# Performance work log

Measured on AMD Instinct MI355X. Metric: run time of the kernel, lower is better.

## Reference

```python
import jax, jax.numpy as jnp
import numpy as np


def setup_inputs() -> dict:
    key = jax.random.key(0)
    k0, k1, k2, k3, k4 = jax.random.split(key, 5)
    B, W, C, C2, D = 4, 64, 512, 512, 64  # D = C // k, k=8
    x = jax.random.normal(k0, (B, W, W, C), dtype=jnp.float32)
    input_h = jax.random.normal(k1, (B, W, W, C2), dtype=jnp.float32)
    f = jax.random.normal(k2, (1, 1, C2, D), dtype=jnp.float32) * 0.02
    g = jax.random.normal(k3, (1, 1, C, D), dtype=jnp.float32) * 0.02
    gamma = jax.random.uniform(k4, (1,), dtype=jnp.float32)
    return {"x": x, "input_h": input_h, "f": f, "g": g, "gamma": gamma}


def reference(x, input_h, f, g, gamma):
    # x: [B,W,W,C] NHWC, input_h: [B,W,W,C2], f: [1,1,C2,D], g: [1,1,C,D]
    B, W, _, C = x.shape
    C2 = input_h.shape[-1]
    N = W * W
    # 1x1 convs == per-pixel channel matmuls
    f_proj = jnp.einsum('bhwc,cd->bhwd', input_h, f[0, 0])  # [B,W,W,D]
    g_proj = jnp.einsum('bhwc,cd->bhwd', x, g[0, 0])        # [B,W,W,D]
    f_flat = f_proj.reshape(B, N, -1)
    g_flat = g_proj.reshape(B, N, -1)
    # unscaled attention scores over spatial positions
    s = jnp.einsum('bnd,bmd->bnm', g_flat, f_flat)          # [B,N,N]
    beta = jax.nn.softmax(s, axis=-1)
    h_flat = input_h.reshape(B, N, C2)
    o = jnp.einsum('bnm,bmc->bnc', beta, h_flat).reshape(B, W, W, C2)
    # mix_concat == 'mix': learned residual mix
    return gamma * o + x
```

## Files before the change

### kernel.cpp

```cpp
#include <hip/hip_runtime.h>
#include <hip/hip_bf16.h>
#include <cstdint>
#include <cstddef>


#define NPOS 4096
#define CCH  512
#define DQK  64
#define LSTR 72

typedef __attribute__((ext_vector_type(8)))  short s8v;
typedef __attribute__((ext_vector_type(4)))  short s4v;
typedef __attribute__((ext_vector_type(4)))  float f4v;

__device__ __forceinline__ float bf2f(unsigned short u) {
    unsigned int x = ((unsigned int)u) << 16;
    return __builtin_bit_cast(float, x);
}
__device__ __forceinline__ unsigned short f2bf(float f) {
    unsigned int u = __builtin_bit_cast(unsigned int, f);
    u += 0x7fffu + ((u >> 16) & 1u);
    return (unsigned short)(u >> 16);
}

__global__ __launch_bounds__(256) void wt_kernel(
    const float* __restrict__ f, const float* __restrict__ g,
    unsigned short* __restrict__ fT, unsigned short* __restrict__ gT)
{
    int gid = blockIdx.x * 256 + threadIdx.x;
    for (int e = 0; e < 4; ++e) {
        int i = e * 16384 + gid;
        int which = i >> 15;
        int j = i & 32767;
        int d = j >> 9, k = j & 511;
        const float* s = which ? g : f;
        unsigned short* dst = which ? gT : fT;
        dst[j] = f2bf(s[k * 64 + d]);
    }
}

__global__ __launch_bounds__(256) void vt_kernel(
    const float* __restrict__ ih, unsigned short* __restrict__ Vt)
{
    __shared__ unsigned short T[64 * 65];
    const int tid = threadIdx.x;
    const int bidx = blockIdx.x;
    const int bb = bidx >> 9;
    const int rem = bidx & 511;
    const int ct = rem >> 6;
    const int nt = rem & 63;

    for (int p = 0; p < 4; ++p) {
        int idx = p * 256 + tid;
        int r = idx >> 4, gg = idx & 15;
        f4v v = *(const f4v*)(ih + ((size_t)bb * NPOS + nt * 64 + r) * CCH + ct * 64 + gg * 4);
        for (int j = 0; j < 4; ++j) T[r * 65 + gg * 4 + j] = f2bf(v[j]);
    }
    __syncthreads();
    for (int p = 0; p < 2; ++p) {
        int idx = p * 256 + tid;
        int c = idx >> 3, ng = idx & 7;
        unsigned short tmp[8];
        for (int j = 0; j < 8; ++j) tmp[j] = T[(ng * 8 + j) * 65 + c];
        *(s8v*)(Vt + ((size_t)bb * CCH + ct * 64 + c) * NPOS + nt * 64 + ng * 8) = *(const s8v*)tmp;
    }
}

__global__ __launch_bounds__(256) void proj_kernel(
    const float* __restrict__ x,  const float* __restrict__ ih,
    const unsigned short* __restrict__ gT, const unsigned short* __restrict__ fT,
    unsigned short* __restrict__ Qg, unsigned short* __restrict__ Kf)
{
    __shared__ __align__(16) short Alds[128 * LSTR];
    __shared__ __align__(16) short Wlds[64 * LSTR];
    const int tid = threadIdx.x;
    const int wave = tid >> 6, lane = tid & 63;
    const int n15 = lane & 15, quad = lane >> 4;
    const int which = blockIdx.x >> 7;
    const int rb = (blockIdx.x & 127) * 128;
    const float* src = which ? ih : x;
    const unsigned short* wT  = which ? fT : gT;
    unsigned short* dst = which ? Kf : Qg;

    f4v acc[2][4];
    for (int i = 0; i < 2; ++i)
        for (int j = 0; j < 4; ++j)
            acc[i][j] = f4v{0.f, 0.f, 0.f, 0.f};

    for (int kc = 0; kc < 8; ++kc) {
        for (int p = 0; p < 8; ++p) {
            int idx = p * 256 + tid;
            int r = idx >> 4, gg = idx & 15;
            f4v v = *(const f4v*)(src + (size_t)(rb + r) * CCH + kc * 64 + gg * 4);
            s4v tv;
            for (int j = 0; j < 4; ++j) tv[j] = (short)f2bf(v[j]);
            *(s4v*)&Alds[r * LSTR + gg * 4] = tv;
        }
        for (int p = 0; p < 2; ++p) {
            int idx = p * 256 + tid;
            int c = idx >> 3, gg = idx & 7;
            *(s8v*)&Wlds[c * LSTR + gg * 8] =
                *(const s8v*)(wT + (size_t)c * CCH + kc * 64 + gg * 8);
        }
        __syncthreads();
        for (int kk = 0; kk < 2; ++kk) {
            s8v af0 = *(const s8v*)&Alds[(wave * 32 +      n15) * LSTR + kk * 32 + quad * 8];
            s8v af1 = *(const s8v*)&Alds[(wave * 32 + 16 + n15) * LSTR + kk * 32 + quad * 8];
            for (int ct = 0; ct < 4; ++ct) {
                s8v bf = *(const s8v*)&Wlds[(ct * 16 + n15) * LSTR + kk * 32 + quad * 8];
                acc[0][ct] = __builtin_amdgcn_mfma_f32_16x16x32_bf16(af0, bf, acc[0][ct], 0, 0, 0);
                acc[1][ct] = __builtin_amdgcn_mfma_f32_16x16x32_bf16(af1, bf, acc[1][ct], 0, 0, 0);
            }
        }
        __syncthreads();
    }
    for (int rt = 0; rt < 2; ++rt)
        for (int ct = 0; ct < 4; ++ct)
            for (int r = 0; r < 4; ++r) {
                int row = wave * 32 + rt * 16 + quad * 4 + r;
                int col = ct * 16 + n15;
                dst[(size_t)(rb + row) * DQK + col] = f2bf(acc[rt][ct][r]);
            }
}

__global__ __launch_bounds__(512) void flash_kernel(
    const unsigned short* __restrict__ Qg,
    const unsigned short* __restrict__ Kf,
    const unsigned short* __restrict__ Vt,
    const float* __restrict__ xin,
    const float* __restrict__ gptr,
    float* __restrict__ out)
{
    __shared__ __align__(16) short Klds[2 * 64 * LSTR];
    __shared__ __align__(16) short Plds[64 * LSTR];
    __shared__ float l_s[64];

    const int tid = threadIdx.x;
    const int wave = tid >> 6;
    const int lane = tid & 63;
    const int n15 = lane & 15, quad = lane >> 4;
    const int bid = blockIdx.x;
    const int xcd = bid & 7;
    const int b = xcd >> 1;
    const int qt = (xcd & 1) + ((bid >> 3) << 1);
    const int qbase = qt * 64;

    const float SOFT_M = 20.0f;
    float lpart = 0.0f;

    f4v acc[4][4];
    for (int i = 0; i < 4; ++i)
        for (int j = 0; j < 4; ++j)
            acc[i][j] = f4v{0.f, 0.f, 0.f, 0.f};

    const int ti = wave >> 1;
    const int mi0 = (wave & 1) * 2;
    s8v qf[2];
    {
        const unsigned short* qp =
            Qg + ((size_t)b * NPOS + qbase + ti * 16 + n15) * DQK + quad * 8;
        qf[0] = *(const s8v*)(qp);
        qf[1] = *(const s8v*)(qp + 32);
    }

    const int cb = wave * 64;
    const unsigned short* Vb = Vt + (size_t)b * CCH * NPOS;

    const int kr = tid >> 3, kg = tid & 7;
    const unsigned short* kbase_p = Kf + ((size_t)b * NPOS + kr) * DQK + kg * 8;
    s8v kreg = *(const s8v*)(kbase_p);

    for (int kb = 0; kb < NPOS / 64; ++kb) {
        const int m0 = kb * 64;
        *(s8v*)&Klds[(kb & 1) * 64 * LSTR + kr * LSTR + kg * 8] = kreg;
        if (kb + 1 < NPOS / 64)
            kreg = *(const s8v*)(kbase_p + (size_t)(m0 + 64) * DQK);
        s8v vf[4][2];
        for (int ct = 0; ct < 4; ++ct) {
            const unsigned short* vp =
                Vb + (size_t)(cb + ct * 16 + n15) * NPOS + m0 + quad * 8;
            vf[ct][0] = *(const s8v*)(vp);
            vf[ct][1] = *(const s8v*)(vp + 32);
        }
        __syncthreads();

        {
            const short* Kb = &Klds[(kb & 1) * 64 * LSTR];
            for (int mm = 0; mm < 2; ++mm) {
                const int mi = mi0 + mm;
                f4v s4 = f4v{0.f, 0.f, 0.f, 0.f};
                for (int ks = 0; ks < 2; ++ks) {
                    s8v kf = *(const s8v*)&Kb[(mi * 16 + n15) * LSTR + ks * 32 + quad * 8];
                    s4 = __builtin_amdgcn_mfma_f32_16x16x32_bf16(qf[ks], kf, s4, 0, 0, 0);
                }
                const int col = mi * 16 + n15;
                const int row0 = ti * 16 + quad * 4;
                for (int r = 0; r < 4; ++r)
                    Plds[(row0 + r) * LSTR + col] =
                        (short)f2bf(__expf(fminf(s4[r], 80.0f) - SOFT_M));
            }
        }
        __syncthreads();

        {
            const int r = tid >> 3, j8 = tid & 7;
            s8v p8 = *(const s8v*)&Plds[r * LSTR + j8 * 8];
            float ls = 0.f;
            for (int e = 0; e < 8; ++e) ls += bf2f((unsigned short)p8[e]);
            lpart += ls;
        }
        for (int kk = 0; kk < 2; ++kk) {
            s8v af[4];
            for (int q4 = 0; q4 < 4; ++q4)
                af[q4] = *(const s8v*)&Plds[(q4 * 16 + n15) * LSTR + kk * 32 + quad * 8];
            for (int q4 = 0; q4 < 4; ++q4)
                for (int ct = 0; ct < 4; ++ct)
                    acc[q4][ct] = __builtin_amdgcn_mfma_f32_16x16x32_bf16(
                        af[q4], vf[ct][kk], acc[q4][ct], 0, 0, 0);
        }
    }

    lpart += __shfl_xor(lpart, 1);
    lpart += __shfl_xor(lpart, 2);
    lpart += __shfl_xor(lpart, 4);
    if ((tid & 7) == 0) l_s[tid >> 3] = lpart;
    __syncthreads();

    const float gamma = gptr[0];
    for (int q4 = 0; q4 < 4; ++q4) {
        for (int r = 0; r < 4; ++r) {
            const int row = q4 * 16 + quad * 4 + r;
            const float sc = gamma / l_s[row];
            for (int ct = 0; ct < 4; ++ct) {
                const int col = cb + ct * 16 + n15;
                const size_t idx = ((size_t)b * NPOS + qbase + row) * CCH + col;
                out[idx] = acc[q4][ct][r] * sc + xin[idx];
            }
        }
    }
}

extern "C" void kernel_launch(void* const* d_in, const int* in_sizes, int n_in,
                              void* d_out, int out_size, void* d_ws, size_t ws_size,
                              hipStream_t stream)
{
    const float* x     = (const float*)d_in[0];
    const float* ih    = (const float*)d_in[1];
    const float* f     = (const float*)d_in[2];
    const float* g     = (const float*)d_in[3];
    const float* gamma = (const float*)d_in[4];
    float* out = (float*)d_out;

    char* ws = (char*)d_ws;
    unsigned short* fT = (unsigned short*)(ws + 0);
    unsigned short* gT = (unsigned short*)(ws + 65536);
    unsigned short* Qg = (unsigned short*)(ws + 131072);
    unsigned short* Kf = (unsigned short*)(ws + 2228224);
    unsigned short* Vt = (unsigned short*)(ws + 4325376);

    wt_kernel<<<64, 256, 0, stream>>>(f, g, fT, gT);
    vt_kernel<<<2048, 256, 0, stream>>>(ih, Vt);
    proj_kernel<<<256, 256, 0, stream>>>(x, ih, gT, fT, Qg, Kf);
    flash_kernel<<<256, 512, 0, stream>>>(Qg, Kf, Vt, x, gamma, out);
}
```

Measured before the change: 277.7 us.

## Split flash kernel over four channel slices to quadruple grid size

```diff
diff --git a/kernel.cpp b/kernel.cpp
--- a/kernel.cpp
+++ b/kernel.cpp
@@ -123,7 +123,7 @@
             }
 }
 
-__global__ __launch_bounds__(512) void flash_kernel(
+__global__ __launch_bounds__(512, 6) void flash_kernel(
     const unsigned short* __restrict__ Qg,
     const unsigned short* __restrict__ Kf,
     const unsigned short* __restrict__ Vt,
@@ -142,16 +142,17 @@
     const int bid = blockIdx.x;
     const int xcd = bid & 7;
     const int b = xcd >> 1;
-    const int qt = (xcd & 1) + ((bid >> 3) << 1);
+    const int rem = bid >> 3;
+    const int cs = rem & 3;
+    const int qt = (xcd & 1) + ((rem >> 2) << 1);
     const int qbase = qt * 64;
 
     const float SOFT_M = 20.0f;
     float lpart = 0.0f;
 
-    f4v acc[4][4];
+    f4v acc[4];
     for (int i = 0; i < 4; ++i)
-        for (int j = 0; j < 4; ++j)
-            acc[i][j] = f4v{0.f, 0.f, 0.f, 0.f};
+        acc[i] = f4v{0.f, 0.f, 0.f, 0.f};
 
     const int ti = wave >> 1;
     const int mi0 = (wave & 1) * 2;
@@ -163,8 +164,9 @@
         qf[1] = *(const s8v*)(qp + 32);
     }
 
-    const int cb = wave * 64;
+    const int cb = cs * 128 + wave * 16;
     const unsigned short* Vb = Vt + (size_t)b * CCH * NPOS;
+    const unsigned short* vrow = Vb + (size_t)(cb + n15) * NPOS + quad * 8;
 
     const int kr = tid >> 3, kg = tid & 7;
     const unsigned short* kbase_p = Kf + ((size_t)b * NPOS + kr) * DQK + kg * 8;
@@ -175,13 +177,9 @@
         *(s8v*)&Klds[(kb & 1) * 64 * LSTR + kr * LSTR + kg * 8] = kreg;
         if (kb + 1 < NPOS / 64)
             kreg = *(const s8v*)(kbase_p + (size_t)(m0 + 64) * DQK);
-        s8v vf[4][2];
-        for (int ct = 0; ct < 4; ++ct) {
-            const unsigned short* vp =
-                Vb + (size_t)(cb + ct * 16 + n15) * NPOS + m0 + quad * 8;
-            vf[ct][0] = *(const s8v*)(vp);
-            vf[ct][1] = *(const s8v*)(vp + 32);
-        }
+        s8v vf[2];
+        vf[0] = *(const s8v*)(vrow + m0);
+        vf[1] = *(const s8v*)(vrow + m0 + 32);
         __syncthreads();
 
         {
@@ -210,13 +208,11 @@
             lpart += ls;
         }
         for (int kk = 0; kk < 2; ++kk) {
-            s8v af[4];
-            for (int q4 = 0; q4 < 4; ++q4)
-                af[q4] = *(const s8v*)&Plds[(q4 * 16 + n15) * LSTR + kk * 32 + quad * 8];
-            for (int q4 = 0; q4 < 4; ++q4)
-                for (int ct = 0; ct < 4; ++ct)
-                    acc[q4][ct] = __builtin_amdgcn_mfma_f32_16x16x32_bf16(
-                        af[q4], vf[ct][kk], acc[q4][ct], 0, 0, 0);
+            for (int q4 = 0; q4 < 4; ++q4) {
+                s8v af = *(const s8v*)&Plds[(q4 * 16 + n15) * LSTR + kk * 32 + quad * 8];
+                acc[q4] = __builtin_amdgcn_mfma_f32_16x16x32_bf16(
+                    af, vf[kk], acc[q4], 0, 0, 0);
+            }
         }
     }
 
@@ -231,11 +227,9 @@
         for (int r = 0; r < 4; ++r) {
             const int row = q4 * 16 + quad * 4 + r;
             const float sc = gamma / l_s[row];
-            for (int ct = 0; ct < 4; ++ct) {
-                const int col = cb + ct * 16 + n15;
-                const size_t idx = ((size_t)b * NPOS + qbase + row) * CCH + col;
-                out[idx] = acc[q4][ct][r] * sc + xin[idx];
-            }
+            const int col = cb + n15;
+            const size_t idx = ((size_t)b * NPOS + qbase + row) * CCH + col;
+            out[idx] = acc[q4][r] * sc + xin[idx];
         }
     }
 }
@@ -261,5 +255,5 @@
     wt_kernel<<<64, 256, 0, stream>>>(f, g, fT, gT);
     vt_kernel<<<2048, 256, 0, stream>>>(ih, Vt);
     proj_kernel<<<256, 256, 0, stream>>>(x, ih, gT, fT, Qg, Kf);
-    flash_kernel<<<256, 512, 0, stream>>>(Qg, Kf, Vt, x, gamma, out);
-}
+    flash_kernel<<<1024, 512, 0, stream>>>(Qg, Kf, Vt, x, gamma, out);
+}
```

Result: slower. 314.8 us (+13.4%).

## Halve query tile to 32 rows, double grid, double-buffer P and drop a barrier

Applied to the files above, without the earlier changes.

```diff
diff --git a/kernel.cpp b/kernel.cpp
--- a/kernel.cpp
+++ b/kernel.cpp
@@ -123,7 +123,7 @@
             }
 }
 
-__global__ __launch_bounds__(512) void flash_kernel(
+__global__ __launch_bounds__(512, 4) void flash_kernel(
     const unsigned short* __restrict__ Qg,
     const unsigned short* __restrict__ Kf,
     const unsigned short* __restrict__ Vt,
@@ -132,8 +132,8 @@
     float* __restrict__ out)
 {
     __shared__ __align__(16) short Klds[2 * 64 * LSTR];
-    __shared__ __align__(16) short Plds[64 * LSTR];
-    __shared__ float l_s[64];
+    __shared__ __align__(16) short Plds[2 * 32 * LSTR];
+    __shared__ float l_s[32];
 
     const int tid = threadIdx.x;
     const int wave = tid >> 6;
@@ -143,18 +143,18 @@
     const int xcd = bid & 7;
     const int b = xcd >> 1;
     const int qt = (xcd & 1) + ((bid >> 3) << 1);
-    const int qbase = qt * 64;
+    const int qbase = qt * 32;
 
     const float SOFT_M = 20.0f;
     float lpart = 0.0f;
 
-    f4v acc[4][4];
-    for (int i = 0; i < 4; ++i)
+    f4v acc[2][4];
+    for (int i = 0; i < 2; ++i)
         for (int j = 0; j < 4; ++j)
             acc[i][j] = f4v{0.f, 0.f, 0.f, 0.f};
 
-    const int ti = wave >> 1;
-    const int mi0 = (wave & 1) * 2;
+    const int ti = wave >> 2;
+    const int mi = wave & 3;
     s8v qf[2];
     {
         const unsigned short* qp =
@@ -165,69 +165,77 @@
 
     const int cb = wave * 64;
     const unsigned short* Vb = Vt + (size_t)b * CCH * NPOS;
+    const unsigned short* vp[4];
+    for (int ct = 0; ct < 4; ++ct)
+        vp[ct] = Vb + (size_t)(cb + ct * 16 + n15) * NPOS + quad * 8;
 
     const int kr = tid >> 3, kg = tid & 7;
     const unsigned short* kbase_p = Kf + ((size_t)b * NPOS + kr) * DQK + kg * 8;
+
     s8v kreg = *(const s8v*)(kbase_p);
+    *(s8v*)&Klds[kr * LSTR + kg * 8] = kreg;
+    kreg = *(const s8v*)(kbase_p + (size_t)64 * DQK);
+    __syncthreads();
 
     for (int kb = 0; kb < NPOS / 64; ++kb) {
         const int m0 = kb * 64;
-        *(s8v*)&Klds[(kb & 1) * 64 * LSTR + kr * LSTR + kg * 8] = kreg;
-        if (kb + 1 < NPOS / 64)
-            kreg = *(const s8v*)(kbase_p + (size_t)(m0 + 64) * DQK);
         s8v vf[4][2];
         for (int ct = 0; ct < 4; ++ct) {
-            const unsigned short* vp =
-                Vb + (size_t)(cb + ct * 16 + n15) * NPOS + m0 + quad * 8;
-            vf[ct][0] = *(const s8v*)(vp);
-            vf[ct][1] = *(const s8v*)(vp + 32);
-        }
-        __syncthreads();
+            vf[ct][0] = *(const s8v*)(vp[ct] + m0);
+            vf[ct][1] = *(const s8v*)(vp[ct] + m0 + 32);
+        }
+        if (kb + 1 < NPOS / 64) {
+            *(s8v*)&Klds[((kb + 1) & 1) * 64 * LSTR + kr * LSTR + kg * 8] = kreg;
+            if (kb + 2 < NPOS / 64)
+                kreg = *(const s8v*)(kbase_p + (size_t)(m0 + 128) * DQK);
+        }
 
         {
             const short* Kb = &Klds[(kb & 1) * 64 * LSTR];
-            for (int mm = 0; mm < 2; ++mm) {
-                const int mi = mi0 + mm;
-                f4v s4 = f4v{0.f, 0.f, 0.f, 0.f};
-                for (int ks = 0; ks < 2; ++ks) {
-                    s8v kf = *(const s8v*)&Kb[(mi * 16 + n15) * LSTR + ks * 32 + quad * 8];
-                    s4 = __builtin_amdgcn_mfma_f32_16x16x32_bf16(qf[ks], kf, s4, 0, 0, 0);
-                }
-                const int col = mi * 16 + n15;
-                const int row0 = ti * 16 + quad * 4;
-                for (int r = 0; r < 4; ++r)
-                    Plds[(row0 + r) * LSTR + col] =
-                        (short)f2bf(__expf(fminf(s4[r], 80.0f) - SOFT_M));
-            }
+            short* Pb = &Plds[(kb & 1) * 32 * LSTR];
+            f4v s4 = f4v{0.f, 0.f, 0.f, 0.f};
+            for (int ks = 0; ks < 2; ++ks) {
+                s8v kf = *(const s8v*)&Kb[(mi * 16 + n15) * LSTR + ks * 32 + quad * 8];
+                s4 = __builtin_amdgcn_mfma_f32_16x16x32_bf16(qf[ks], kf, s4, 0, 0, 0);
+            }
+            const int col = mi * 16 + n15;
+            const int row0 = ti * 16 + quad * 4;
+            for (int r = 0; r < 4; ++r)
+                Pb[(row0 + r) * LSTR + col] =
+                    (short)f2bf(__expf(fminf(s4[r], 80.0f) - SOFT_M));
         }
         __syncthreads();
 
         {
-            const int r = tid >> 3, j8 = tid & 7;
-            s8v p8 = *(const s8v*)&Plds[r * LSTR + j8 * 8];
-            float ls = 0.f;
-            for (int e = 0; e < 8; ++e) ls += bf2f((unsigned short)p8[e]);
-            lpart += ls;
-        }
-        for (int kk = 0; kk < 2; ++kk) {
-            s8v af[4];
-            for (int q4 = 0; q4 < 4; ++q4)
-                af[q4] = *(const s8v*)&Plds[(q4 * 16 + n15) * LSTR + kk * 32 + quad * 8];
-            for (int q4 = 0; q4 < 4; ++q4)
-                for (int ct = 0; ct < 4; ++ct)
-                    acc[q4][ct] = __builtin_amdgcn_mfma_f32_16x16x32_bf16(
-                        af[q4], vf[ct][kk], acc[q4][ct], 0, 0, 0);
+            const short* Pb = &Plds[(kb & 1) * 32 * LSTR];
+            {
+                const int r = tid >> 4, g4 = tid & 15;
+                s4v p4 = *(const s4v*)&Pb[r * LSTR + g4 * 4];
+                float ls = 0.f;
+                for (int e = 0; e < 4; ++e) ls += bf2f((unsigned short)p4[e]);
+                lpart += ls;
+            }
+            for (int kk = 0; kk < 2; ++kk) {
+                s8v af[2];
+                for (int q4 = 0; q4 < 2; ++q4)
+                    af[q4] = *(const s8v*)&Pb[(q4 * 16 + n15) * LSTR + kk * 32 + quad * 8];
+                for (int q4 = 0; q4 < 2; ++q4)
+                    for (int ct = 0; ct < 4; ++ct)
+                        acc[q4][ct] = __builtin_amdgcn_mfma_f32_16x16x32_bf16(
+                            af[q4], vf[ct][kk], acc[q4][ct], 0, 0, 0);
+            }
         }
     }
 
     lpart += __shfl_xor(lpart, 1);
     lpart += __shfl_xor(lpart, 2);
     lpart += __shfl_xor(lpart, 4);
-    if ((tid & 7) == 0) l_s[tid >> 3] = lpart;
+    lpart += __shfl_xor(lpart, 8);
+    if ((tid & 15) == 0) l_s[tid >> 4] = lpart;
     __syncthreads();
 
     const float gamma = gptr[0];
-    for (int q4 = 0; q4 < 4; ++q4) {
+    for (int q4 = 0; q4 < 2; ++q4) {
         for (int r = 0; r < 4; ++r) {
             const int row = q4 * 16 + quad * 4 + r;
             const float sc = gamma / l_s[row];
@@ -261,5 +269,5 @@
     wt_kernel<<<64, 256, 0, stream>>>(f, g, fT, gT);
     vt_kernel<<<2048, 256, 0, stream>>>(ih, Vt);
     proj_kernel<<<256, 256, 0, stream>>>(x, ih, gT, fT, Qg, Kf);
-    flash_kernel<<<256, 512, 0, stream>>>(Qg, Kf, Vt, x, gamma, out);
-}
+    flash_kernel<<<512, 512, 0, stream>>>(Qg, Kf, Vt, x, gamma, out);
+}
```

Result: slower. 384.7 us (+38.5%).
